# Kernel optimization log

Measured on AMD Instinct MI355X. Metric: run time of the kernel, lower is better.

Reference implementation:

```python
import jax, jax.numpy as jnp
import numpy as np

B, S, D, H, O, E, K = 4, 1024, 1024, 2048, 1024, 8, 2
LOAD_BALANCE_WEIGHT = 0.01


def setup_inputs() -> dict:
    key = jax.random.key(0)
    ks = jax.random.split(key, 9)
    scale = 0.02
    return {
        "x": jax.random.normal(ks[0], (B, S, D), jnp.float32),
        "Wg": scale * jax.random.normal(ks[1], (D, E), jnp.float32),
        "bg": jnp.zeros((E,), jnp.float32),
        "W1": scale * jax.random.normal(ks[2], (E, D, H), jnp.float32),
        "b1": jnp.zeros((E, H), jnp.float32),
        "W2": scale * jax.random.normal(ks[3], (E, H, H), jnp.float32),
        "b2": jnp.zeros((E, H), jnp.float32),
        "W3": scale * jax.random.normal(ks[4], (E, H, O), jnp.float32),
        "b3": jnp.zeros((E, O), jnp.float32),
    }


def reference(x, Wg, bg, W1, b1, W2, b2, W3, b3):
    # Eval-mode MoE: no gating noise, dropout is identity.
    b, s, d = x.shape
    e = Wg.shape[1]

    # --- gating: noisy top-k gating (noise off in eval) ---
    raw_gates = x @ Wg + bg                         # [B,S,E]
    topk_logits, topk_idx = jax.lax.top_k(raw_gates, K)  # [B,S,K]
    gates = jax.nn.softmax(topk_logits, axis=-1)    # [B,S,K]

    # Combine weights per expert: scatter top-k gates into [B,S,E].
    onehot = jax.nn.one_hot(topk_idx, e, dtype=x.dtype)      # [B,S,K,E]
    combine = jnp.sum(onehot * gates[..., None], axis=-2)    # [B,S,E]

    # --- expert MLPs (dense grouped GEMM over all tokens) ---
    xt = x.reshape(-1, d)            # [T,D]
    wt = combine.reshape(-1, e)      # [T,E]
    h = jax.nn.relu(jnp.einsum('td,edh->eth', xt, W1) + b1[:, None, :])
    h = jax.nn.relu(jnp.einsum('eth,ehg->etg', h, W2) + b2[:, None, :])
    y = jnp.einsum('eth,eho->eto', h, W3) + b3[:, None, :]   # [E,T,O]
    out = jnp.einsum('te,eto->to', wt, y).reshape(b, s, -1)  # [B,S,O]

    # --- auxiliary losses ---
    gate_probs = jax.nn.softmax(raw_gates, axis=-1)          # [B,S,E]
    avg_gate_probs = gate_probs.mean(axis=(0, 1))            # [E]
    avg_expert_counts = combine.mean(axis=(0, 1))            # [E]
    load_balance_loss = LOAD_BALANCE_WEIGHT * e * jnp.sum(avg_gate_probs * avg_expert_counts)
    gate_entropy = -jnp.sum(avg_gate_probs * jnp.log(avg_gate_probs + 1e-8))

    return out, load_balance_loss, avg_expert_counts, gate_entropy
```

## Files before the change

### kernel.cpp

```cpp
#include <hip/hip_runtime.h>
#include <hip/hip_bf16.h>
#include <math.h>

#define T_TOK 4096
#define D_IN  1024
#define H_DIM 2048
#define O_DIM 1024
#define NE    8
#define ROWCAP 9216
#define RT128  72

typedef __bf16 bf16x8 __attribute__((ext_vector_type(8)));
typedef __bf16 bf16x4 __attribute__((ext_vector_type(4)));
typedef float  f32x4  __attribute__((ext_vector_type(4)));

#define ELT(f, j) ((j) == 0 ? (f).x : (j) == 1 ? (f).y : (j) == 2 ? (f).z : (f).w)

__device__ __forceinline__ void gl_lds16(const void* g, void* l) {
    __builtin_amdgcn_global_load_lds(
        (const __attribute__((address_space(1))) void*)g,
        (__attribute__((address_space(3))) void*)l, 16, 0, 0);
}

__global__ __launch_bounds__(256) void gating_kernel(
    const float* __restrict__ x, const float* __restrict__ Wg, const float* __restrict__ bg,
    __bf16* __restrict__ xb, float* __restrict__ gates_tk, int* __restrict__ idx_tk,
    int* __restrict__ counts, double* __restrict__ prob_part, double* __restrict__ gsum_part)
{
    __shared__ float WgS[8][1032];
    __shared__ float bgS[NE];
    __shared__ double tok_p[32][NE];
    __shared__ double tok_g[32][2];
    __shared__ int    tok_i[32][2];
    const int tid = threadIdx.x;

    for (int i = tid; i < D_IN * NE; i += 256)
        WgS[i >> 10][i & 1023] = Wg[i];
    if (tid < NE) bgS[tid] = bg[tid];

    {
        const size_t base = (size_t)blockIdx.x * 32 * D_IN;
        for (int i = tid * 4; i < 32 * D_IN; i += 256 * 4) {
            float4 v = *(const float4*)(x + base + i);
            bf16x4 b = {(__bf16)v.x, (__bf16)v.y, (__bf16)v.z, (__bf16)v.w};
            *(bf16x4*)(xb + base + i) = b;
        }
    }
    __syncthreads();

    const int tokL = tid >> 3;
    const int part = tid & 7;
    const int t = blockIdx.x * 32 + tokL;
    const float* xr = x + (size_t)t * D_IN + part * 128;

    double s[NE] = {0, 0, 0, 0, 0, 0, 0, 0};
    for (int j = 0; j < 128; j += 4) {
        float4 xv = *(const float4*)(xr + j);
        const float* w = &WgS[part][j * 8];
        #pragma unroll
        for (int jj = 0; jj < 4; ++jj) {
            double xd = (double)(ELT(xv, jj));
            #pragma unroll
            for (int e = 0; e < NE; ++e)
                s[e] += xd * (double)w[jj * 8 + e];
        }
    }
    #pragma unroll
    for (int off = 4; off; off >>= 1)
        #pragma unroll
        for (int e = 0; e < NE; ++e)
            s[e] += __shfl_xor(s[e], off);

    if (part == 0) {
        double rg[NE];
        #pragma unroll
        for (int e = 0; e < NE; ++e) rg[e] = s[e] + (double)bgS[e];
        int i0 = 0;
        #pragma unroll
        for (int e = 1; e < NE; ++e) if (rg[e] > rg[i0]) i0 = e;
        int i1 = -1;
        #pragma unroll
        for (int e = 0; e < NE; ++e) {
            if (e == i0) continue;
            if (i1 < 0 || rg[e] > rg[i1]) i1 = e;
        }
        double e1 = exp(rg[i1] - rg[i0]);
        double den = 1.0 + e1;
        gates_tk[t * 2] = (float)(1.0 / den); gates_tk[t * 2 + 1] = (float)(e1 / den);
        idx_tk[t * 2] = i0;   idx_tk[t * 2 + 1] = i1;
        tok_g[tokL][0] = 1.0 / den; tok_g[tokL][1] = e1 / den;
        tok_i[tokL][0] = i0;        tok_i[tokL][1] = i1;
        double mx = rg[0];
        #pragma unroll
        for (int e = 1; e < NE; ++e) mx = fmax(mx, rg[e]);
        double pe[NE], sum = 0.0;
        #pragma unroll
        for (int e = 0; e < NE; ++e) { pe[e] = exp(rg[e] - mx); sum += pe[e]; }
        #pragma unroll
        for (int e = 0; e < NE; ++e) tok_p[tokL][e] = pe[e] / sum;
    }
    __syncthreads();
    if (tid < NE) {
        double p = 0.0, g = 0.0; int c = 0;
        for (int i = 0; i < 32; ++i) {
            p += tok_p[i][tid];
            if (tok_i[i][0] == tid) { g += tok_g[i][0]; ++c; }
            if (tok_i[i][1] == tid) { g += tok_g[i][1]; ++c; }
        }
        prob_part[blockIdx.x * NE + tid] = p;
        gsum_part[blockIdx.x * NE + tid] = g;
        atomicAdd(&counts[tid], c);
    }
}

__global__ void build_offsets(const int* __restrict__ counts, int* __restrict__ poffset,
                              int* __restrict__ totalp, int* __restrict__ token_ids)
{
    __shared__ int po[NE + 1];
    __shared__ int cnt[NE];
    const int tid = threadIdx.x;
    if (tid == 0) {
        po[0] = 0;
        for (int e = 0; e < NE; ++e) {
            cnt[e] = counts[e];
            int pc = (cnt[e] + 127) & ~127;
            po[e + 1] = po[e] + pc;
        }
        for (int e = 0; e <= NE; ++e) poffset[e] = po[e];
        totalp[0] = po[NE];
    }
    __syncthreads();
    for (int e = 0; e < NE; ++e) {
        int base = po[e], c = cnt[e], pc = po[e + 1] - po[e];
        for (int i = c + tid; i < pc; i += 64) token_ids[base + i] = 0;
    }
}

__global__ __launch_bounds__(256) void scatter_rows(
    const int* __restrict__ idx_tk, const int* __restrict__ poffset,
    int* __restrict__ cursors, int* __restrict__ token_ids, int* __restrict__ t2r)
{
    int t = blockIdx.x * 256 + threadIdx.x;
    if (t >= T_TOK) return;
    for (int k = 0; k < 2; ++k) {
        int e = idx_tk[t * 2 + k];
        int pos = atomicAdd(&cursors[e], 1);
        int r = poffset[e] + pos;
        token_ids[r] = t;
        t2r[t * 2 + k] = r;
    }
}

template<bool GATHER, bool RELU, bool OUTBF16>
__global__ __launch_bounds__(256) void gemm_expert(
    const __bf16* __restrict__ A, int lda,
    const float* __restrict__ Bw, int Kdim, int N,
    const float* __restrict__ bias,
    void* __restrict__ Out, int ldo,
    const int* __restrict__ token_ids,
    const int* __restrict__ poffset,
    const int* __restrict__ totalp)
{
    __shared__ __bf16 As[128 * 64];
    __shared__ __bf16 Bs[128 * 64];
    const int tid = threadIdx.x;
    const int row0 = blockIdx.y * 128;
    if (row0 >= totalp[0]) return;
    int e = 0;
    while (e < NE - 1 && row0 >= poffset[e + 1]) ++e;
    const int n0 = blockIdx.x * 128;
    const float* Be = Bw + (size_t)e * Kdim * N;
    const float* biase = bias + (size_t)e * N;

    const int srow = tid >> 3;
    const int jperm = (tid & 7) ^ (srow & 7);
    const int scol = jperm * 8;
    int arow_g[4];
    #pragma unroll
    for (int c = 0; c < 4; ++c) {
        int r = row0 + c * 32 + srow;
        arow_g[c] = GATHER ? token_ids[r] : r;
    }

    const int rg = tid >> 5;
    const int cB = tid & 31;
    const float* bsrc0 = Be + (size_t)rg * 8 * N + n0 + cB * 4;

    const int lane = tid & 63;
    const int quad = lane >> 4;
    const int m16  = lane & 15;
    const int wave = tid >> 6;
    const int wm = wave >> 1, wn = wave & 1;

    f32x4 acc[4][4];
    #pragma unroll
    for (int i = 0; i < 4; ++i)
        #pragma unroll
        for (int j = 0; j < 4; ++j)
            acc[i][j] = (f32x4){0.f, 0.f, 0.f, 0.f};

    const int niter = Kdim >> 6;

    float4 r[8];
    #pragma unroll
    for (int i = 0; i < 8; ++i)
        r[i] = *(const float4*)(bsrc0 + (size_t)i * N);

    for (int kt = 0; kt < niter; ++kt) {
        const int kofs = kt * 64 + scol;
        #pragma unroll
        for (int c = 0; c < 4; ++c)
            gl_lds16(A + (size_t)arow_g[c] * lda + kofs, (char*)As + c * 4096 + tid * 16);
        #pragma unroll
        for (int j = 0; j < 4; ++j) {
            const int n = cB * 4 + j;
            bf16x8 v;
            #pragma unroll
            for (int i = 0; i < 8; ++i) v[i] = (__bf16)(ELT(r[i], j));
            *(bf16x8*)&Bs[n * 64 + ((rg ^ (n & 7)) << 3)] = v;
        }
        __syncthreads();
        if (kt + 1 < niter) {
            const float* bsrc = bsrc0 + (size_t)(kt + 1) * 64 * N;
            #pragma unroll
            for (int i = 0; i < 8; ++i)
                r[i] = *(const float4*)(bsrc + (size_t)i * N);
        }
        #pragma unroll
        for (int ks = 0; ks < 2; ++ks) {
            const int p = ((ks << 2) | quad) ^ (m16 & 7);
            bf16x8 af[4], bfr[4];
            #pragma unroll
            for (int i = 0; i < 4; ++i)
                af[i] = *(const bf16x8*)&As[(wm * 64 + i * 16 + m16) * 64 + p * 8];
            #pragma unroll
            for (int j = 0; j < 4; ++j)
                bfr[j] = *(const bf16x8*)&Bs[(wn * 64 + j * 16 + m16) * 64 + p * 8];
            #pragma unroll
            for (int i = 0; i < 4; ++i)
                #pragma unroll
                for (int j = 0; j < 4; ++j)
                    acc[i][j] = __builtin_amdgcn_mfma_f32_16x16x32_bf16(af[i], bfr[j], acc[i][j], 0, 0, 0);
        }
        __syncthreads();
    }
    #pragma unroll
    for (int i = 0; i < 4; ++i)
        #pragma unroll
        for (int j = 0; j < 4; ++j)
            #pragma unroll
            for (int rr = 0; rr < 4; ++rr) {
                int grow = row0 + wm * 64 + i * 16 + quad * 4 + rr;
                int gcol = n0 + wn * 64 + j * 16 + m16;
                float v = acc[i][j][rr] + biase[gcol];
                if (RELU) v = v > 0.f ? v : 0.f;
                if (OUTBF16) ((__bf16*)Out)[(size_t)grow * ldo + gcol] = (__bf16)v;
                else         ((float*)Out)[(size_t)grow * ldo + gcol] = v;
            }
}

__global__ __launch_bounds__(256) void combine_out(
    const float* __restrict__ y, const float* __restrict__ gates_tk,
    const int* __restrict__ t2r, float* __restrict__ out)
{
    const int t = blockIdx.x;
    const int o = threadIdx.x * 4;
    const int r0 = t2r[t * 2], r1 = t2r[t * 2 + 1];
    const float g0 = gates_tk[t * 2], g1 = gates_tk[t * 2 + 1];
    float4 a = *(const float4*)&y[(size_t)r0 * O_DIM + o];
    float4 b = *(const float4*)&y[(size_t)r1 * O_DIM + o];
    float4 c;
    c.x = g0 * a.x + g1 * b.x;
    c.y = g0 * a.y + g1 * b.y;
    c.z = g0 * a.z + g1 * b.z;
    c.w = g0 * a.w + g1 * b.w;
    *(float4*)&out[(size_t)t * O_DIM + o] = c;
}

__global__ void finalize_kernel(const double* __restrict__ prob_part,
                                const double* __restrict__ gsum_part,
                                float* __restrict__ out)
{
    __shared__ double ps[NE], gs[NE];
    const int tid = threadIdx.x;
    if (tid < NE) {
        double p = 0.0, g = 0.0;
        for (int b = 0; b < 128; ++b) {
            p += prob_part[b * NE + tid];
            g += gsum_part[b * NE + tid];
        }
        ps[tid] = p / (double)T_TOK;
        gs[tid] = g / (double)T_TOK;
        out[(size_t)T_TOK * O_DIM + 1 + tid] = (float)(g / (double)T_TOK);
    }
    __syncthreads();
    if (tid == 0) {
        double lb = 0.0, ent = 0.0;
        for (int e = 0; e < NE; ++e) {
            lb += ps[e] * gs[e];
            ent -= ps[e] * log(ps[e] + 1e-8);
        }
        out[(size_t)T_TOK * O_DIM] = (float)(0.01 * 8.0 * lb);
        out[(size_t)T_TOK * O_DIM + 9] = (float)ent;
    }
}

extern "C" void kernel_launch(void* const* d_in, const int* in_sizes, int n_in,
                              void* d_out, int out_size, void* d_ws, size_t ws_size,
                              hipStream_t stream)
{
    const float* x  = (const float*)d_in[0];
    const float* Wg = (const float*)d_in[1];
    const float* bg = (const float*)d_in[2];
    const float* W1 = (const float*)d_in[3];
    const float* b1 = (const float*)d_in[4];
    const float* W2 = (const float*)d_in[5];
    const float* b2 = (const float*)d_in[6];
    const float* W3 = (const float*)d_in[7];
    const float* b3 = (const float*)d_in[8];
    float* out = (float*)d_out;
    char* ws = (char*)d_ws;

    size_t off = 0;
    __bf16* xb  = (__bf16*)(ws + off); off += (size_t)T_TOK * D_IN * 2;
    __bf16* h1  = (__bf16*)(ws + off);
    float*  y   = (float*) (ws + off); off += (size_t)ROWCAP * H_DIM * 2;
    __bf16* h2  = (__bf16*)(ws + off); off += (size_t)ROWCAP * H_DIM * 2;
    float* gates_tk = (float*)(ws + off); off += T_TOK * 2 * 4;
    int* idx_tk     = (int*)(ws + off);   off += T_TOK * 2 * 4;
    int* t2r        = (int*)(ws + off);   off += T_TOK * 2 * 4;
    int* token_ids  = (int*)(ws + off);   off += ROWCAP * 4;
    double* prob_part = (double*)(ws + off); off += 128 * NE * 8;
    double* gsum_part = (double*)(ws + off); off += 128 * NE * 8;
    char* small     = ws + off;
    int* counts     = (int*)(small + 0);
    int* cursors    = (int*)(small + 32);
    int* poffset    = (int*)(small + 64);
    int* totalp     = (int*)(small + 112);

    hipMemsetAsync(small, 0, 256, stream);
    gating_kernel<<<128, 256, 0, stream>>>(x, Wg, bg, xb, gates_tk, idx_tk,
                                           counts, prob_part, gsum_part);
    build_offsets<<<1, 64, 0, stream>>>(counts, poffset, totalp, token_ids);
    scatter_rows<<<16, 256, 0, stream>>>(idx_tk, poffset, cursors, token_ids, t2r);
    gemm_expert<true,  true,  true ><<<dim3(H_DIM / 128, RT128), 256, 0, stream>>>(
        xb, D_IN, W1, D_IN, H_DIM, b1, (void*)h1, H_DIM, token_ids, poffset, totalp);
    gemm_expert<false, true,  true ><<<dim3(H_DIM / 128, RT128), 256, 0, stream>>>(
        h1, H_DIM, W2, H_DIM, H_DIM, b2, (void*)h2, H_DIM, token_ids, poffset, totalp);
    gemm_expert<false, false, false><<<dim3(O_DIM / 128, RT128), 256, 0, stream>>>(
        h2, H_DIM, W3, H_DIM, O_DIM, b3, (void*)y, O_DIM, token_ids, poffset, totalp);
    combine_out<<<T_TOK, 256, 0, stream>>>(y, gates_tk, t2r, out);
    finalize_kernel<<<1, 64, 0, stream>>>(prob_part, gsum_part, out);
}
```

Before: 631.3 us.

## Pre-convert expert weights to bf16 and remap GEMM blocks across XCDs

Adds a conversion kernel that turns W1/W2/W3 from fp32 into bf16 workspace copies once per call, so the expert GEMMs read half as many weight bytes and no longer convert in the inner loop. The GEMM block index is remapped so that blocks landing on the same XCD share weight column tiles, aiming for better L2 reuse. The B-tile LDS swizzle is changed to reduce bank conflicts. The conversion pass itself reads all fp32 weights and writes bf16 copies on every call, and that extra traffic may offset part of the savings.

```diff
diff --git a/kernel.cpp b/kernel.cpp
--- a/kernel.cpp
+++ b/kernel.cpp
@@ -110,6 +110,25 @@
         prob_part[blockIdx.x * NE + tid] = p;
         gsum_part[blockIdx.x * NE + tid] = g;
         atomicAdd(&counts[tid], c);
+    }
+}
+
+__global__ __launch_bounds__(256) void cvt_weights(
+    const float* __restrict__ W1, const float* __restrict__ W2, const float* __restrict__ W3,
+    __bf16* __restrict__ W1b, __bf16* __restrict__ W2b, __bf16* __restrict__ W3b)
+{
+    const float* src; __bf16* dst; int n8;
+    if (blockIdx.z == 0)      { src = W1; dst = W1b; n8 = (NE * D_IN * H_DIM) / 8; }
+    else if (blockIdx.z == 1) { src = W2; dst = W2b; n8 = (NE * H_DIM * H_DIM) / 8; }
+    else                      { src = W3; dst = W3b; n8 = (NE * H_DIM * O_DIM) / 8; }
+    int i = blockIdx.x * 256 + threadIdx.x;
+    const int stride = gridDim.x * 256;
+    for (; i < n8; i += stride) {
+        float4 a = ((const float4*)src)[(size_t)2 * i];
+        float4 b = ((const float4*)src)[(size_t)2 * i + 1];
+        bf16x8 v = {(__bf16)a.x, (__bf16)a.y, (__bf16)a.z, (__bf16)a.w,
+                    (__bf16)b.x, (__bf16)b.y, (__bf16)b.z, (__bf16)b.w};
+        *(bf16x8*)(dst + (size_t)i * 8) = v;
     }
 }
 
@@ -154,7 +173,7 @@
 template<bool GATHER, bool RELU, bool OUTBF16>
 __global__ __launch_bounds__(256) void gemm_expert(
     const __bf16* __restrict__ A, int lda,
-    const float* __restrict__ Bw, int Kdim, int N,
+    const __bf16* __restrict__ Bw, int Kdim, int N,
     const float* __restrict__ bias,
     void* __restrict__ Out, int ldo,
     const int* __restrict__ token_ids,
@@ -164,12 +183,19 @@
     __shared__ __bf16 As[128 * 64];
     __shared__ __bf16 Bs[128 * 64];
     const int tid = threadIdx.x;
-    const int row0 = blockIdx.y * 128;
+
+    const int NYg = gridDim.y;
+    const int flat = blockIdx.y * gridDim.x + blockIdx.x;
+    const int xcd = flat & 7, idx = flat >> 3;
+    const int lbx = xcd + 8 * (idx / NYg);
+    const int lby = idx % NYg;
+
+    const int row0 = lby * 128;
     if (row0 >= totalp[0]) return;
     int e = 0;
     while (e < NE - 1 && row0 >= poffset[e + 1]) ++e;
-    const int n0 = blockIdx.x * 128;
-    const float* Be = Bw + (size_t)e * Kdim * N;
+    const int n0 = lbx * 128;
+    const __bf16* Be = Bw + (size_t)e * Kdim * N;
     const float* biase = bias + (size_t)e * N;
 
     const int srow = tid >> 3;
@@ -184,7 +210,7 @@
 
     const int rg = tid >> 5;
     const int cB = tid & 31;
-    const float* bsrc0 = Be + (size_t)rg * 8 * N + n0 + cB * 4;
+    const __bf16* bsrc0 = Be + (size_t)rg * 8 * N + n0 + cB * 4;
 
     const int lane = tid & 63;
     const int quad = lane >> 4;
@@ -201,10 +227,10 @@
 
     const int niter = Kdim >> 6;
 
-    float4 r[8];
+    bf16x4 r[8];
     #pragma unroll
     for (int i = 0; i < 8; ++i)
-        r[i] = *(const float4*)(bsrc0 + (size_t)i * N);
+        r[i] = *(const bf16x4*)(bsrc0 + (size_t)i * N);
 
     for (int kt = 0; kt < niter; ++kt) {
         const int kofs = kt * 64 + scol;
@@ -214,28 +240,32 @@
         #pragma unroll
         for (int j = 0; j < 4; ++j) {
             const int n = cB * 4 + j;
+            const int key = (n & 7) ^ ((n >> 4) & 3);
             bf16x8 v;
             #pragma unroll
-            for (int i = 0; i < 8; ++i) v[i] = (__bf16)(ELT(r[i], j));
-            *(bf16x8*)&Bs[n * 64 + ((rg ^ (n & 7)) << 3)] = v;
+            for (int i = 0; i < 8; ++i) v[i] = r[i][j];
+            *(bf16x8*)&Bs[n * 64 + ((rg ^ key) << 3)] = v;
         }
         __syncthreads();
         if (kt + 1 < niter) {
-            const float* bsrc = bsrc0 + (size_t)(kt + 1) * 64 * N;
+            const __bf16* bsrc = bsrc0 + (size_t)(kt + 1) * 64 * N;
             #pragma unroll
             for (int i = 0; i < 8; ++i)
-                r[i] = *(const float4*)(bsrc + (size_t)i * N);
+                r[i] = *(const bf16x4*)(bsrc + (size_t)i * N);
         }
         #pragma unroll
         for (int ks = 0; ks < 2; ++ks) {
-            const int p = ((ks << 2) | quad) ^ (m16 & 7);
+            const int c0 = (ks << 2) | quad;
+            const int pA = c0 ^ (m16 & 7);
             bf16x8 af[4], bfr[4];
             #pragma unroll
             for (int i = 0; i < 4; ++i)
-                af[i] = *(const bf16x8*)&As[(wm * 64 + i * 16 + m16) * 64 + p * 8];
-            #pragma unroll
-            for (int j = 0; j < 4; ++j)
-                bfr[j] = *(const bf16x8*)&Bs[(wn * 64 + j * 16 + m16) * 64 + p * 8];
+                af[i] = *(const bf16x8*)&As[(wm * 64 + i * 16 + m16) * 64 + pA * 8];
+            #pragma unroll
+            for (int j = 0; j < 4; ++j) {
+                const int pB = pA ^ j;
+                bfr[j] = *(const bf16x8*)&Bs[(wn * 64 + j * 16 + m16) * 64 + pB * 8];
+            }
             #pragma unroll
             for (int i = 0; i < 4; ++i)
                 #pragma unroll
@@ -326,6 +356,9 @@
     __bf16* h1  = (__bf16*)(ws + off);
     float*  y   = (float*) (ws + off); off += (size_t)ROWCAP * H_DIM * 2;
     __bf16* h2  = (__bf16*)(ws + off); off += (size_t)ROWCAP * H_DIM * 2;
+    __bf16* W1b = (__bf16*)(ws + off); off += (size_t)NE * D_IN * H_DIM * 2;
+    __bf16* W2b = (__bf16*)(ws + off); off += (size_t)NE * H_DIM * H_DIM * 2;
+    __bf16* W3b = (__bf16*)(ws + off); off += (size_t)NE * H_DIM * O_DIM * 2;
     float* gates_tk = (float*)(ws + off); off += T_TOK * 2 * 4;
     int* idx_tk     = (int*)(ws + off);   off += T_TOK * 2 * 4;
     int* t2r        = (int*)(ws + off);   off += T_TOK * 2 * 4;
@@ -341,14 +374,15 @@
     hipMemsetAsync(small, 0, 256, stream);
     gating_kernel<<<128, 256, 0, stream>>>(x, Wg, bg, xb, gates_tk, idx_tk,
                                            counts, prob_part, gsum_part);
+    cvt_weights<<<dim3(1024, 1, 3), 256, 0, stream>>>(W1, W2, W3, W1b, W2b, W3b);
     build_offsets<<<1, 64, 0, stream>>>(counts, poffset, totalp, token_ids);
     scatter_rows<<<16, 256, 0, stream>>>(idx_tk, poffset, cursors, token_ids, t2r);
     gemm_expert<true,  true,  true ><<<dim3(H_DIM / 128, RT128), 256, 0, stream>>>(
-        xb, D_IN, W1, D_IN, H_DIM, b1, (void*)h1, H_DIM, token_ids, poffset, totalp);
+        xb, D_IN, W1b, D_IN, H_DIM, b1, (void*)h1, H_DIM, token_ids, poffset, totalp);
     gemm_expert<false, true,  true ><<<dim3(H_DIM / 128, RT128), 256, 0, stream>>>(
-        h1, H_DIM, W2, H_DIM, H_DIM, b2, (void*)h2, H_DIM, token_ids, poffset, totalp);
+        h1, H_DIM, W2b, H_DIM, H_DIM, b2, (void*)h2, H_DIM, token_ids, poffset, totalp);
     gemm_expert<false, false, false><<<dim3(O_DIM / 128, RT128), 256, 0, stream>>>(
-        h2, H_DIM, W3, H_DIM, O_DIM, b3, (void*)y, O_DIM, token_ids, poffset, totalp);
+        h2, H_DIM, W3b, H_DIM, O_DIM, b3, (void*)y, O_DIM, token_ids, poffset, totalp);
     combine_out<<<T_TOK, 256, 0, stream>>>(y, gates_tk, t2r, out);
     finalize_kernel<<<1, 64, 0, stream>>>(prob_part, gsum_part, out);
 }
```

After: 669.7 us. 6.1% more time.

## Fuse routing kernels with deterministic scan, fold finalize into combine, reswizzle B tile

Applied to the files above, without the earlier changes.

Replaces the atomic count, offset-build and atomic scatter kernels with one route_tokens kernel. It derives per-expert offsets from per-block counts and assigns rows with a packed 16-bit-per-expert prefix scan, which also removes the memset. The loss finalization moves into block 0 of combine_out, so two fewer launches run. The B-tile LDS swizzle now also XORs with the 16-row group index to cut bank conflicts on B fragment reads, at the cost of slightly more index arithmetic.

```diff
diff --git a/kernel.cpp b/kernel.cpp
--- a/kernel.cpp
+++ b/kernel.cpp
@@ -25,7 +25,7 @@
 __global__ __launch_bounds__(256) void gating_kernel(
     const float* __restrict__ x, const float* __restrict__ Wg, const float* __restrict__ bg,
     __bf16* __restrict__ xb, float* __restrict__ gates_tk, int* __restrict__ idx_tk,
-    int* __restrict__ counts, double* __restrict__ prob_part, double* __restrict__ gsum_part)
+    int* __restrict__ cnt_part, double* __restrict__ prob_part, double* __restrict__ gsum_part)
 {
     __shared__ float WgS[8][1032];
     __shared__ float bgS[NE];
@@ -109,45 +109,70 @@
         }
         prob_part[blockIdx.x * NE + tid] = p;
         gsum_part[blockIdx.x * NE + tid] = g;
-        atomicAdd(&counts[tid], c);
-    }
-}
-
-__global__ void build_offsets(const int* __restrict__ counts, int* __restrict__ poffset,
-                              int* __restrict__ totalp, int* __restrict__ token_ids)
-{
+        cnt_part[blockIdx.x * NE + tid] = c;
+    }
+}
+
+__global__ __launch_bounds__(256) void route_tokens(
+    const int* __restrict__ cnt_part, const int* __restrict__ idx_tk,
+    int* __restrict__ poffset, int* __restrict__ totalp,
+    int* __restrict__ token_ids, int* __restrict__ t2r)
+{
+    __shared__ int cntE[NE], baseE[NE];
     __shared__ int po[NE + 1];
-    __shared__ int cnt[NE];
+    __shared__ int4 sb[256];
     const int tid = threadIdx.x;
+    const int b = blockIdx.x;
+
+    if (tid < NE) {
+        int tot = 0, pre = 0;
+        for (int g = 0; g < 128; ++g) {
+            int v = cnt_part[g * NE + tid];
+            tot += v;
+            if (g < b * 8) pre += v;
+        }
+        cntE[tid] = tot;
+        baseE[tid] = pre;
+    }
+    __syncthreads();
     if (tid == 0) {
         po[0] = 0;
-        for (int e = 0; e < NE; ++e) {
-            cnt[e] = counts[e];
-            int pc = (cnt[e] + 127) & ~127;
-            po[e + 1] = po[e] + pc;
-        }
-        for (int e = 0; e <= NE; ++e) poffset[e] = po[e];
-        totalp[0] = po[NE];
-    }
-    __syncthreads();
+        for (int e = 0; e < NE; ++e) po[e + 1] = po[e] + ((cntE[e] + 127) & ~127);
+        if (b == 0) {
+            for (int e = 0; e <= NE; ++e) poffset[e] = po[e];
+            totalp[0] = po[NE];
+        }
+    }
+    __syncthreads();
+
+    const int t = b * 256 + tid;
+    const int e0 = idx_tk[t * 2], e1 = idx_tk[t * 2 + 1];
+    int4 p = {0, 0, 0, 0};
+    ((int*)&p)[e0 >> 1] += 1 << ((e0 & 1) * 16);
+    ((int*)&p)[e1 >> 1] += 1 << ((e1 & 1) * 16);
+    sb[tid] = p;
+    __syncthreads();
+    for (int off = 1; off < 256; off <<= 1) {
+        int4 v = sb[tid];
+        int4 u = {0, 0, 0, 0};
+        if (tid >= off) u = sb[tid - off];
+        __syncthreads();
+        v.x += u.x; v.y += u.y; v.z += u.z; v.w += u.w;
+        sb[tid] = v;
+        __syncthreads();
+    }
+    int4 inc = sb[tid];
+    {
+        int pos0 = ((((const int*)&inc)[e0 >> 1] >> ((e0 & 1) * 16)) & 0xffff) - 1;
+        int r0 = po[e0] + baseE[e0] + pos0;
+        token_ids[r0] = t; t2r[t * 2] = r0;
+        int pos1 = ((((const int*)&inc)[e1 >> 1] >> ((e1 & 1) * 16)) & 0xffff) - 1;
+        int r1 = po[e1] + baseE[e1] + pos1;
+        token_ids[r1] = t; t2r[t * 2 + 1] = r1;
+    }
     for (int e = 0; e < NE; ++e) {
-        int base = po[e], c = cnt[e], pc = po[e + 1] - po[e];
-        for (int i = c + tid; i < pc; i += 64) token_ids[base + i] = 0;
-    }
-}
-
-__global__ __launch_bounds__(256) void scatter_rows(
-    const int* __restrict__ idx_tk, const int* __restrict__ poffset,
-    int* __restrict__ cursors, int* __restrict__ token_ids, int* __restrict__ t2r)
-{
-    int t = blockIdx.x * 256 + threadIdx.x;
-    if (t >= T_TOK) return;
-    for (int k = 0; k < 2; ++k) {
-        int e = idx_tk[t * 2 + k];
-        int pos = atomicAdd(&cursors[e], 1);
-        int r = poffset[e] + pos;
-        token_ids[r] = t;
-        t2r[t * 2 + k] = r;
+        int c = cntE[e], base = po[e], pc = po[e + 1] - po[e];
+        for (int i = c + b * 256 + tid; i < pc; i += 16 * 256) token_ids[base + i] = 0;
     }
 }
 
@@ -214,10 +239,11 @@
         #pragma unroll
         for (int j = 0; j < 4; ++j) {
             const int n = cB * 4 + j;
+            const int key = (n & 7) ^ ((n >> 4) & 3);
             bf16x8 v;
             #pragma unroll
             for (int i = 0; i < 8; ++i) v[i] = (__bf16)(ELT(r[i], j));
-            *(bf16x8*)&Bs[n * 64 + ((rg ^ (n & 7)) << 3)] = v;
+            *(bf16x8*)&Bs[n * 64 + ((rg ^ key) << 3)] = v;
         }
         __syncthreads();
         if (kt + 1 < niter) {
@@ -228,14 +254,17 @@
         }
         #pragma unroll
         for (int ks = 0; ks < 2; ++ks) {
-            const int p = ((ks << 2) | quad) ^ (m16 & 7);
+            const int c0 = (ks << 2) | quad;
+            const int pA = c0 ^ (m16 & 7);
             bf16x8 af[4], bfr[4];
             #pragma unroll
             for (int i = 0; i < 4; ++i)
-                af[i] = *(const bf16x8*)&As[(wm * 64 + i * 16 + m16) * 64 + p * 8];
-            #pragma unroll
-            for (int j = 0; j < 4; ++j)
-                bfr[j] = *(const bf16x8*)&Bs[(wn * 64 + j * 16 + m16) * 64 + p * 8];
+                af[i] = *(const bf16x8*)&As[(wm * 64 + i * 16 + m16) * 64 + pA * 8];
+            #pragma unroll
+            for (int j = 0; j < 4; ++j) {
+                const int pB = pA ^ j;
+                bfr[j] = *(const bf16x8*)&Bs[(wn * 64 + j * 16 + m16) * 64 + pB * 8];
+            }
             #pragma unroll
             for (int i = 0; i < 4; ++i)
                 #pragma unroll
@@ -261,7 +290,8 @@
 
 __global__ __launch_bounds__(256) void combine_out(
     const float* __restrict__ y, const float* __restrict__ gates_tk,
-    const int* __restrict__ t2r, float* __restrict__ out)
+    const int* __restrict__ t2r, float* __restrict__ out,
+    const double* __restrict__ prob_part, const double* __restrict__ gsum_part)
 {
     const int t = blockIdx.x;
     const int o = threadIdx.x * 4;
@@ -275,33 +305,30 @@
     c.z = g0 * a.z + g1 * b.z;
     c.w = g0 * a.w + g1 * b.w;
     *(float4*)&out[(size_t)t * O_DIM + o] = c;
-}
-
-__global__ void finalize_kernel(const double* __restrict__ prob_part,
-                                const double* __restrict__ gsum_part,
-                                float* __restrict__ out)
-{
-    __shared__ double ps[NE], gs[NE];
-    const int tid = threadIdx.x;
-    if (tid < NE) {
-        double p = 0.0, g = 0.0;
-        for (int b = 0; b < 128; ++b) {
-            p += prob_part[b * NE + tid];
-            g += gsum_part[b * NE + tid];
-        }
-        ps[tid] = p / (double)T_TOK;
-        gs[tid] = g / (double)T_TOK;
-        out[(size_t)T_TOK * O_DIM + 1 + tid] = (float)(g / (double)T_TOK);
-    }
-    __syncthreads();
-    if (tid == 0) {
-        double lb = 0.0, ent = 0.0;
-        for (int e = 0; e < NE; ++e) {
-            lb += ps[e] * gs[e];
-            ent -= ps[e] * log(ps[e] + 1e-8);
-        }
-        out[(size_t)T_TOK * O_DIM] = (float)(0.01 * 8.0 * lb);
-        out[(size_t)T_TOK * O_DIM + 9] = (float)ent;
+
+    if (blockIdx.x == 0) {
+        __shared__ double ps[NE], gs[NE];
+        const int tid = threadIdx.x;
+        if (tid < NE) {
+            double p = 0.0, g = 0.0;
+            for (int bb = 0; bb < 128; ++bb) {
+                p += prob_part[bb * NE + tid];
+                g += gsum_part[bb * NE + tid];
+            }
+            ps[tid] = p / (double)T_TOK;
+            gs[tid] = g / (double)T_TOK;
+            out[(size_t)T_TOK * O_DIM + 1 + tid] = (float)(g / (double)T_TOK);
+        }
+        __syncthreads();
+        if (tid == 0) {
+            double lb = 0.0, ent = 0.0;
+            for (int e = 0; e < NE; ++e) {
+                lb += ps[e] * gs[e];
+                ent -= ps[e] * log(ps[e] + 1e-8);
+            }
+            out[(size_t)T_TOK * O_DIM] = (float)(0.01 * 8.0 * lb);
+            out[(size_t)T_TOK * O_DIM + 9] = (float)ent;
+        }
     }
 }
 
@@ -332,23 +359,18 @@
     int* token_ids  = (int*)(ws + off);   off += ROWCAP * 4;
     double* prob_part = (double*)(ws + off); off += 128 * NE * 8;
     double* gsum_part = (double*)(ws + off); off += 128 * NE * 8;
-    char* small     = ws + off;
-    int* counts     = (int*)(small + 0);
-    int* cursors    = (int*)(small + 32);
-    int* poffset    = (int*)(small + 64);
-    int* totalp     = (int*)(small + 112);
-
-    hipMemsetAsync(small, 0, 256, stream);
+    int* cnt_part   = (int*)(ws + off);   off += 128 * NE * 4;
+    int* poffset    = (int*)(ws + off);   off += (NE + 1) * 4;
+    int* totalp     = (int*)(ws + off);   off += 16;
+
     gating_kernel<<<128, 256, 0, stream>>>(x, Wg, bg, xb, gates_tk, idx_tk,
-                                           counts, prob_part, gsum_part);
-    build_offsets<<<1, 64, 0, stream>>>(counts, poffset, totalp, token_ids);
-    scatter_rows<<<16, 256, 0, stream>>>(idx_tk, poffset, cursors, token_ids, t2r);
+                                           cnt_part, prob_part, gsum_part);
+    route_tokens<<<16, 256, 0, stream>>>(cnt_part, idx_tk, poffset, totalp, token_ids, t2r);
     gemm_expert<true,  true,  true ><<<dim3(H_DIM / 128, RT128), 256, 0, stream>>>(
         xb, D_IN, W1, D_IN, H_DIM, b1, (void*)h1, H_DIM, token_ids, poffset, totalp);
     gemm_expert<false, true,  true ><<<dim3(H_DIM / 128, RT128), 256, 0, stream>>>(
         h1, H_DIM, W2, H_DIM, H_DIM, b2, (void*)h2, H_DIM, token_ids, poffset, totalp);
     gemm_expert<false, false, false><<<dim3(O_DIM / 128, RT128), 256, 0, stream>>>(
         h2, H_DIM, W3, H_DIM, O_DIM, b3, (void*)y, O_DIM, token_ids, poffset, totalp);
-    combine_out<<<T_TOK, 256, 0, stream>>>(y, gates_tk, t2r, out);
-    finalize_kernel<<<1, 64, 0, stream>>>(prob_part, gsum_part, out);
-}
+    combine_out<<<T_TOK, 256, 0, stream>>>(y, gates_tk, t2r, out, prob_part, gsum_part);
+}
```

New measurement: 574.2 us. 1.1x faster.
